# Optimization experiments

Hardware: AMD Instinct MI355X
Metric: run time of the kernel (lower is better)

## Reference

```python
import jax, jax.numpy as jnp
import numpy as np

N = 100000   # nodes
E = 1600000  # edges (avg degree 16)
G = 512      # graphs in batch
IN = 96      # in_channels
H = 128      # hidden_channels
C = 100      # num_classes
ED = 8       # edge_dim
L = 4        # num_layers
EPS_LN = 1e-5


def setup_inputs() -> dict:
    key = jax.random.key(0)
    ks = jax.random.split(key, 24)
    s = 0.05
    d = {
        "x": jax.random.normal(ks[0], (N, IN), jnp.float32),
        "edge_index": jax.random.randint(ks[1], (2, E), 0, N, jnp.int32),
        "batch": jnp.sort(jax.random.randint(ks[2], (N,), 0, G, jnp.int32)),
        "edge_attr": jax.random.normal(ks[3], (E, ED), jnp.float32),
        # edge encoder MLP: Linear(ED,H) -> ReLU -> Linear(H,1)
        "ee_W1": jax.random.normal(ks[4], (ED, H), jnp.float32) * s,
        "ee_b1": jnp.zeros((H,), jnp.float32),
        "ee_W2": jax.random.normal(ks[5], (H, 1), jnp.float32) * s,
        "ee_b2": jnp.zeros((1,), jnp.float32),
        # GCNConv weights (PyG: lin without bias, bias added after aggregation)
        "W0": jax.random.normal(ks[6], (IN, H), jnp.float32) * s,
        "cb0": jnp.zeros((H,), jnp.float32),
        "W1": jax.random.normal(ks[7], (H, H), jnp.float32) * s,
        "cb1": jnp.zeros((H,), jnp.float32),
        "W2": jax.random.normal(ks[8], (H, H), jnp.float32) * s,
        "cb2": jnp.zeros((H,), jnp.float32),
        "W3": jax.random.normal(ks[9], (H, H), jnp.float32) * s,
        "cb3": jnp.zeros((H,), jnp.float32),
        # LayerNorm params
        "g0": jnp.ones((H,), jnp.float32), "be0": jnp.zeros((H,), jnp.float32),
        "g1": jnp.ones((H,), jnp.float32), "be1": jnp.zeros((H,), jnp.float32),
        "g2": jnp.ones((H,), jnp.float32), "be2": jnp.zeros((H,), jnp.float32),
        "g3": jnp.ones((H,), jnp.float32), "be3": jnp.zeros((H,), jnp.float32),
        # residual projection for layer 0 only (IN != H)
        "res_W": jax.random.normal(ks[10], (IN, H), jnp.float32) * s,
        "res_b": jnp.zeros((H,), jnp.float32),
        # head: Linear(2H,H) -> ReLU -> Linear(H,C)
        "hW1": jax.random.normal(ks[11], (2 * H, H), jnp.float32) * s,
        "hb1": jnp.zeros((H,), jnp.float32),
        "hW2": jax.random.normal(ks[12], (H, C), jnp.float32) * s,
        "hb2": jnp.zeros((C,), jnp.float32),
    }
    return d


def _layer_norm(h, g, b):
    mu = jnp.mean(h, axis=-1, keepdims=True)
    var = jnp.mean(jnp.square(h - mu), axis=-1, keepdims=True)
    return g * (h - mu) / jnp.sqrt(var + EPS_LN) + b


def reference(x, edge_index, batch, edge_attr,
              ee_W1, ee_b1, ee_W2, ee_b2,
              W0, cb0, W1, cb1, W2, cb2, W3, cb3,
              g0, be0, g1, be1, g2, be2, g3, be3,
              res_W, res_b, hW1, hb1, hW2, hb2):
    row, col = edge_index[0], edge_index[1]

    # edge weight = softplus(MLP(edge_attr)) + 1e-4  -> [E]
    eh = jax.nn.relu(edge_attr @ ee_W1 + ee_b1)
    ew = jax.nn.softplus((eh @ ee_W2 + ee_b2)[:, 0]) + 1e-4

    # add self loops with weight 1 (PyG GCNConv default)
    loops = jnp.arange(N, dtype=row.dtype)
    row_sl = jnp.concatenate([row, loops])
    col_sl = jnp.concatenate([col, loops])
    ew_sl = jnp.concatenate([ew, jnp.ones((N,), ew.dtype)])

    # symmetric normalization: D^-1/2 A D^-1/2 (deg over target index)
    deg = jax.ops.segment_sum(ew_sl, col_sl, num_segments=N)
    dis = jnp.where(deg > 0, jax.lax.rsqrt(deg), 0.0)
    norm = dis[row_sl] * ew_sl * dis[col_sl]  # [E+N]

    def conv(h, W, b):
        hw = h @ W                                   # [N,H]
        msg = hw[row_sl] * norm[:, None]             # [E+N,H]
        return jax.ops.segment_sum(msg, col_sl, num_segments=N) + b

    Ws = [W0, W1, W2, W3]
    cbs = [cb0, cb1, cb2, cb3]
    gs = [g0, g1, g2, g3]
    bes = [be0, be1, be2, be3]

    hidden = []
    cur = x
    for i in range(L):
        h = conv(cur, Ws[i], cbs[i])
        h = _layer_norm(h, gs[i], bes[i])
        res = cur @ res_W + res_b if i == 0 else cur
        h = jax.nn.relu(h + res)
        # dropout: eval mode -> identity
        hidden.append(h)
        cur = h
    xm = jnp.mean(jnp.stack(hidden, axis=0), axis=0)  # [N,H]

    # meanmax pooling over graphs
    counts = jax.ops.segment_sum(jnp.ones((N,), xm.dtype), batch, num_segments=G)
    gmean = jax.ops.segment_sum(xm, batch, num_segments=G) / jnp.maximum(counts, 1.0)[:, None]
    gmax = jax.ops.segment_max(xm, batch, num_segments=G)
    gmax = jnp.where(jnp.isfinite(gmax), gmax, 0.0)
    g = jnp.concatenate([gmean, gmax], axis=-1)       # [G,2H]

    # head (dropout identity in eval)
    return jax.nn.relu(g @ hW1 + hb1) @ hW2 + hb2     # [G,C]
```

## Files before the change

kernel.cpp:

```cpp
#include <hip/hip_runtime.h>
#include <hip/hip_fp16.h>
#include <math.h>

#define NN 100000
#define EE 1600000
#define GB 512
#define INC 96
#define HH 128
#define CC 100
#define MAXD 64
#define BUCKB 9
#define NBUK 196
#define CAPB 10240
#define EB 4096

typedef __bf16 bf16x8 __attribute__((ext_vector_type(8)));
typedef _Float16 f16x8 __attribute__((ext_vector_type(8)));
typedef float f32x4 __attribute__((ext_vector_type(4)));

__device__ __forceinline__ float unpack_w_f32(unsigned v) {
    return __half2float(__ushort_as_half((unsigned short)(v & 0x7FFFu)));
}
__device__ __forceinline__ __half2 unpack_w_h2(unsigned v) {
    __half h = __ushort_as_half((unsigned short)(v & 0x7FFFu));
    return __halves2half2(h, h);
}

__global__ __launch_bounds__(512) void k_prep(
    const float* __restrict__ W0, const float* __restrict__ resW,
    const float* __restrict__ W1m, const float* __restrict__ W2m, const float* __restrict__ W3m,
    const float* __restrict__ eeW1,
    __half* __restrict__ wt0, __half* __restrict__ wtR,
    __half* __restrict__ wt1, __half* __restrict__ wt2, __half* __restrict__ wt3,
    __bf16* __restrict__ w1f)
{
    int tid = threadIdx.x;
    if (blockIdx.x == 288) {
        int t = tid >> 6, lane = tid & 63;
        int ln15 = lane & 15, quad = lane >> 4;
        bf16x8 v = {};
        if (quad == 0) {
#pragma unroll
            for (int j = 0; j < 8; ++j) v[j] = (__bf16)eeW1[j * 128 + t * 16 + ln15];
        }
        *(bf16x8*)&w1f[(size_t)(t * 64 + lane) * 8] = v;
        return;
    }
    if (tid >= 256) return;
    int idx = blockIdx.x * 256 + tid;
    const float* src; __half* dst; int K, base;
    if (idx < 12288)      { src = W0;   dst = wt0; K = 96;  base = 0; }
    else if (idx < 24576) { src = resW; dst = wtR; K = 96;  base = 12288; }
    else if (idx < 40960) { src = W1m;  dst = wt1; K = 128; base = 24576; }
    else if (idx < 57344) { src = W2m;  dst = wt2; K = 128; base = 40960; }
    else if (idx < 73728) { src = W3m;  dst = wt3; K = 128; base = 57344; }
    else return;
    int l = idx - base;
    int k = l >> 7, n = l & 127;
    dst[(size_t)n * K + k] = __float2half(src[l]);
}

__global__ __launch_bounds__(256) void k_edge_mlp_mfma(
    const float* __restrict__ ea,
    const __bf16* __restrict__ w1f, const float* __restrict__ b1,
    const float* __restrict__ W2, const float* __restrict__ b2,
    __half* __restrict__ ew)
{
    __shared__ float sDot[128];
    int tid = threadIdx.x, wva = tid >> 6, lane = tid & 63;
    int ln15 = lane & 15, quad = lane >> 4;
    int ebase = blockIdx.x * 128 + wva * 32;

    bf16x8 bfr[8];
#pragma unroll
    for (int t = 0; t < 8; ++t) bfr[t] = *(const bf16x8*)&w1f[(size_t)(t * 64 + lane) * 8];

    bf16x8 a0 = {}, a1 = {};
    if (quad == 0) {
        const float* p0 = &ea[(size_t)(ebase + ln15) * 8];
        float4 u0 = *(const float4*)p0, u1 = *(const float4*)(p0 + 4);
        a0[0] = (__bf16)u0.x; a0[1] = (__bf16)u0.y; a0[2] = (__bf16)u0.z; a0[3] = (__bf16)u0.w;
        a0[4] = (__bf16)u1.x; a0[5] = (__bf16)u1.y; a0[6] = (__bf16)u1.z; a0[7] = (__bf16)u1.w;
        const float* p1 = &ea[(size_t)(ebase + 16 + ln15) * 8];
        float4 w0 = *(const float4*)p1, w1v = *(const float4*)(p1 + 4);
        a1[0] = (__bf16)w0.x; a1[1] = (__bf16)w0.y; a1[2] = (__bf16)w0.z; a1[3] = (__bf16)w0.w;
        a1[4] = (__bf16)w1v.x; a1[5] = (__bf16)w1v.y; a1[6] = (__bf16)w1v.z; a1[7] = (__bf16)w1v.w;
    }

    f32x4 d0 = {0.f, 0.f, 0.f, 0.f}, d1 = {0.f, 0.f, 0.f, 0.f};
#pragma unroll
    for (int t = 0; t < 8; ++t) {
        f32x4 z = {0.f, 0.f, 0.f, 0.f};
        f32x4 c0 = __builtin_amdgcn_mfma_f32_16x16x32_bf16(a0, bfr[t], z, 0, 0, 0);
        f32x4 c1 = __builtin_amdgcn_mfma_f32_16x16x32_bf16(a1, bfr[t], z, 0, 0, 0);
        int col = t * 16 + ln15;
        float b1v = b1[col], w2v = W2[col];
#pragma unroll
        for (int r = 0; r < 4; ++r) {
            float v0 = fmaxf(c0[r] + b1v, 0.0f);
            float v1 = fmaxf(c1[r] + b1v, 0.0f);
            d0[r] = fmaf(v0, w2v, d0[r]);
            d1[r] = fmaf(v1, w2v, d1[r]);
        }
    }
#pragma unroll
    for (int o = 1; o < 16; o <<= 1) {
#pragma unroll
        for (int r = 0; r < 4; ++r) {
            d0[r] += __shfl_xor(d0[r], o, 64);
            d1[r] += __shfl_xor(d1[r], o, 64);
        }
    }
    if (ln15 == 0) {
#pragma unroll
        for (int r = 0; r < 4; ++r) {
            sDot[wva * 32 + quad * 4 + r]      = d0[r];
            sDot[wva * 32 + 16 + quad * 4 + r] = d1[r];
        }
    }
    __syncthreads();
    if (tid < 128) {
        int e = blockIdx.x * 128 + tid;
        float x = sDot[tid] + b2[0];
        float sp = (x > 20.0f) ? x : log1pf(expf(x));
        ew[e] = __float2half(sp + 1e-4f);
    }
}

__global__ __launch_bounds__(256) void k_split(const int* __restrict__ ei, const __half* __restrict__ ew,
                                               int* __restrict__ cntB, uint2* __restrict__ barr) {
    __shared__ unsigned hist[NBUK];
    __shared__ unsigned gbase[NBUK];
    __shared__ unsigned short rloc[EB];
    int tid = threadIdx.x;
    for (int b = tid; b < NBUK; b += 256) hist[b] = 0;
    __syncthreads();
    int e0 = blockIdx.x * EB;
#pragma unroll
    for (int j = 0; j < EB / 256; ++j) {
        int e = e0 + j * 256 + tid;
        if (e < EE) {
            int c = ei[EE + e];
            rloc[j * 256 + tid] = (unsigned short)atomicAdd(&hist[c >> BUCKB], 1u);
        }
    }
    __syncthreads();
    for (int b = tid; b < NBUK; b += 256)
        gbase[b] = (hist[b] > 0) ? (unsigned)atomicAdd(&cntB[b], (int)hist[b]) : 0u;
    __syncthreads();
#pragma unroll
    for (int j = 0; j < EB / 256; ++j) {
        int e = e0 + j * 256 + tid;
        if (e < EE) {
            int c = ei[EE + e];
            int b = c >> BUCKB;
            unsigned pos = gbase[b] + rloc[j * 256 + tid];
            if (pos < CAPB) {
                unsigned hb = (unsigned)__half_as_ushort(ew[e]) & 0x7FFFu;
                barr[(size_t)b * CAPB + pos] = make_uint2(((unsigned)c << 15) | hb, (unsigned)ei[e]);
            }
        }
    }
}

__global__ __launch_bounds__(256) void k_build(const int* __restrict__ cntB, const uint2* __restrict__ barr,
                                               unsigned* __restrict__ epack, int* __restrict__ cnt,
                                               float* __restrict__ dis) {
    __shared__ unsigned ncnt[512];
    __shared__ float ndeg[512];
    int tid = threadIdx.x, b = blockIdx.x;
    for (int i = tid; i < 512; i += 256) { ncnt[i] = 0; ndeg[i] = 0.0f; }
    __syncthreads();
    int n0 = b << BUCKB;
    int m = cntB[b]; if (m > CAPB) m = CAPB;
    for (int i = tid; i < m; i += 256) {
        uint2 rec = barr[(size_t)b * CAPB + i];
        int c = (int)(rec.x >> 15);
        int cl = c - n0;
        unsigned rank = atomicAdd(&ncnt[cl], 1u);
        if (rank < MAXD) epack[(size_t)c * MAXD + rank] = (rec.y << 15) | (rec.x & 0x7FFFu);
        atomicAdd(&ndeg[cl], unpack_w_f32(rec.x));
    }
    __syncthreads();
    int nn = NN - n0; if (nn > 512) nn = 512;
    for (int i = tid; i < nn; i += 256) {
        unsigned cc = ncnt[i]; if (cc > MAXD) cc = MAXD;
        cnt[n0 + i] = (int)cc;
        dis[n0 + i] = rsqrtf(1.0f + ndeg[i]);
    }
}

__global__ __launch_bounds__(256) void k_gemm_f16(
    const __half* __restrict__ A, const __half* __restrict__ Bt,
    const float* __restrict__ dis, __half* __restrict__ C, int M, int K)
{
    int tid = threadIdx.x;
    int wv = tid >> 6, lane = tid & 63;
    int ln15 = lane & 15, quad = lane >> 4;
    int m0 = blockIdx.x * 64;
    int n0 = wv * 32;
    f32x4 acc[4][2];
#pragma unroll
    for (int mt = 0; mt < 4; ++mt)
#pragma unroll
        for (int nt = 0; nt < 2; ++nt) acc[mt][nt] = (f32x4){0.f, 0.f, 0.f, 0.f};

    int rowm[4];
#pragma unroll
    for (int mt = 0; mt < 4; ++mt) {
        int r = m0 + mt * 16 + ln15;
        rowm[mt] = r < M ? r : M - 1;
    }
    for (int kc = 0; kc < K; kc += 32) {
        f16x8 af[4], bfr[2];
#pragma unroll
        for (int mt = 0; mt < 4; ++mt)
            af[mt] = *(const f16x8*)&A[(size_t)rowm[mt] * K + kc + quad * 8];
#pragma unroll
        for (int nt = 0; nt < 2; ++nt)
            bfr[nt] = *(const f16x8*)&Bt[(size_t)(n0 + nt * 16 + ln15) * K + kc + quad * 8];
#pragma unroll
        for (int mt = 0; mt < 4; ++mt)
#pragma unroll
            for (int nt = 0; nt < 2; ++nt)
                acc[mt][nt] = __builtin_amdgcn_mfma_f32_16x16x32_f16(af[mt], bfr[nt], acc[mt][nt], 0, 0, 0);
    }
#pragma unroll
    for (int nt = 0; nt < 2; ++nt) {
        int col = n0 + nt * 16 + ln15;
#pragma unroll
        for (int mt = 0; mt < 4; ++mt) {
#pragma unroll
            for (int r = 0; r < 4; ++r) {
                int row = m0 + mt * 16 + quad * 4 + r;
                if (row < M) C[(size_t)row * 128 + col] = __float2half(acc[mt][nt][r] * dis[row]);
            }
        }
    }
}

__global__ __launch_bounds__(256) void k_gemm_dual(
    const float* __restrict__ A, const __half* __restrict__ Bt1, const __half* __restrict__ Bt2,
    const float* __restrict__ bias2, const float* __restrict__ dis,
    __half* __restrict__ C1, __half* __restrict__ C2, int M, int K)
{
    int tid = threadIdx.x;
    int wv = tid >> 6, lane = tid & 63;
    int ln15 = lane & 15, quad = lane >> 4;
    int m0 = blockIdx.x * 64;
    int n0 = wv * 32;
    f32x4 acc1[4][2], acc2[4][2];
#pragma unroll
    for (int mt = 0; mt < 4; ++mt)
#pragma unroll
        for (int nt = 0; nt < 2; ++nt) {
            acc1[mt][nt] = (f32x4){0.f, 0.f, 0.f, 0.f};
            acc2[mt][nt] = (f32x4){0.f, 0.f, 0.f, 0.f};
        }
    int rowm[4];
#pragma unroll
    for (int mt = 0; mt < 4; ++mt) {
        int r = m0 + mt * 16 + ln15;
        rowm[mt] = r < M ? r : M - 1;
    }
    for (int kc = 0; kc < K; kc += 32) {
        f16x8 af[4], bf1[2], bf2[2];
#pragma unroll
        for (int mt = 0; mt < 4; ++mt) {
            const float* ap = &A[(size_t)rowm[mt] * K + kc + quad * 8];
            float4 u0 = *(const float4*)ap, u1 = *(const float4*)(ap + 4);
            af[mt][0] = (_Float16)u0.x; af[mt][1] = (_Float16)u0.y;
            af[mt][2] = (_Float16)u0.z; af[mt][3] = (_Float16)u0.w;
            af[mt][4] = (_Float16)u1.x; af[mt][5] = (_Float16)u1.y;
            af[mt][6] = (_Float16)u1.z; af[mt][7] = (_Float16)u1.w;
        }
#pragma unroll
        for (int nt = 0; nt < 2; ++nt) {
            bf1[nt] = *(const f16x8*)&Bt1[(size_t)(n0 + nt * 16 + ln15) * K + kc + quad * 8];
            bf2[nt] = *(const f16x8*)&Bt2[(size_t)(n0 + nt * 16 + ln15) * K + kc + quad * 8];
        }
#pragma unroll
        for (int mt = 0; mt < 4; ++mt)
#pragma unroll
            for (int nt = 0; nt < 2; ++nt) {
                acc1[mt][nt] = __builtin_amdgcn_mfma_f32_16x16x32_f16(af[mt], bf1[nt], acc1[mt][nt], 0, 0, 0);
                acc2[mt][nt] = __builtin_amdgcn_mfma_f32_16x16x32_f16(af[mt], bf2[nt], acc2[mt][nt], 0, 0, 0);
            }
    }
#pragma unroll
    for (int nt = 0; nt < 2; ++nt) {
        int col = n0 + nt * 16 + ln15;
        float bv2 = bias2[col];
#pragma unroll
        for (int mt = 0; mt < 4; ++mt) {
#pragma unroll
            for (int r = 0; r < 4; ++r) {
                int row = m0 + mt * 16 + quad * 4 + r;
                if (row < M) {
                    C1[(size_t)row * 128 + col] = __float2half(acc1[mt][nt][r] * dis[row]);
                    C2[(size_t)row * 128 + col] = __float2half(acc2[mt][nt][r] + bv2);
                }
            }
        }
    }
}

__global__ __launch_bounds__(256) void k_agg_ln(
    const __half* __restrict__ hw, const float* __restrict__ dis,
    const int* __restrict__ cnt, const unsigned* __restrict__ epack,
    const float* __restrict__ cb, const float* __restrict__ gam,
    const float* __restrict__ bet, const __half* __restrict__ res,
    __half* __restrict__ out, int n)
{
    int wv = threadIdx.x >> 6;
    int lane = threadIdx.x & 63;
    int i = blockIdx.x * 4 + wv;
    if (i >= n) return;
    float di = dis[i];
    __half2 acca = *(const __half2*)&hw[(size_t)i * HH + lane * 2];
    __half2 accb = __halves2half2(__float2half(0.0f), __float2half(0.0f));
    int cn = cnt[i];
    const unsigned* ebase = &epack[(size_t)i * MAXD];
    int k = 0;
    for (; k + 8 <= cn; k += 8) {
        uint4 q0 = *(const uint4*)&ebase[k];
        uint4 q1 = *(const uint4*)&ebase[k + 4];
        __half2 v0 = *(const __half2*)&hw[(size_t)(q0.x >> 15) * HH + lane * 2];
        __half2 v1 = *(const __half2*)&hw[(size_t)(q0.y >> 15) * HH + lane * 2];
        __half2 v2 = *(const __half2*)&hw[(size_t)(q0.z >> 15) * HH + lane * 2];
        __half2 v3 = *(const __half2*)&hw[(size_t)(q0.w >> 15) * HH + lane * 2];
        __half2 v4 = *(const __half2*)&hw[(size_t)(q1.x >> 15) * HH + lane * 2];
        __half2 v5 = *(const __half2*)&hw[(size_t)(q1.y >> 15) * HH + lane * 2];
        __half2 v6 = *(const __half2*)&hw[(size_t)(q1.z >> 15) * HH + lane * 2];
        __half2 v7 = *(const __half2*)&hw[(size_t)(q1.w >> 15) * HH + lane * 2];
        acca = __hfma2(v0, unpack_w_h2(q0.x), acca);
        accb = __hfma2(v4, unpack_w_h2(q1.x), accb);
        acca = __hfma2(v1, unpack_w_h2(q0.y), acca);
        accb = __hfma2(v5, unpack_w_h2(q1.y), accb);
        acca = __hfma2(v2, unpack_w_h2(q0.z), acca);
        accb = __hfma2(v6, unpack_w_h2(q1.z), accb);
        acca = __hfma2(v3, unpack_w_h2(q0.w), acca);
        accb = __hfma2(v7, unpack_w_h2(q1.w), accb);
    }
    for (; k < cn; ++k) {
        unsigned e = ebase[k];
        __half2 v = *(const __half2*)&hw[(size_t)(e >> 15) * HH + lane * 2];
        acca = __hfma2(v, unpack_w_h2(e), acca);
    }
    __half2 acc = __hadd2(acca, accb);
    float2 af = __half22float2(acc);
    float2 cbv = *(const float2*)&cb[lane * 2];
    af.x = fmaf(di, af.x, cbv.x);
    af.y = fmaf(di, af.y, cbv.y);
    float s1 = af.x + af.y;
    float s2 = af.x * af.x + af.y * af.y;
#pragma unroll
    for (int o = 32; o > 0; o >>= 1) {
        s1 += __shfl_xor(s1, o, 64);
        s2 += __shfl_xor(s2, o, 64);
    }
    float mean = s1 * (1.0f / HH);
    float var = fmaxf(s2 * (1.0f / HH) - mean * mean, 0.0f);
    float rstd = rsqrtf(var + 1e-5f);
    float2 gv = *(const float2*)&gam[lane * 2];
    float2 bv = *(const float2*)&bet[lane * 2];
    float2 rv = __half22float2(*(const __half2*)&res[(size_t)i * HH + lane * 2]);
    float hx = fmaxf(fmaf(gv.x, (af.x - mean) * rstd, bv.x) + rv.x, 0.0f);
    float hy = fmaxf(fmaf(gv.y, (af.y - mean) * rstd, bv.y) + rv.y, 0.0f);
    *(__half2*)&out[(size_t)i * HH + lane * 2] = __floats2half2_rn(hx, hy);
}

__global__ __launch_bounds__(512) void k_pool_head(
    const __half* __restrict__ l0, const __half* __restrict__ l1,
    const __half* __restrict__ l2, const __half* __restrict__ l3,
    const int* __restrict__ batch,
    const float* __restrict__ hW1, const float* __restrict__ hb1,
    const float* __restrict__ hW2, const float* __restrict__ hb2,
    float* __restrict__ out, int n)
{
    __shared__ float ssum[8][128];
    __shared__ float smax[8][128];
    __shared__ __align__(16) float sg[256];
    __shared__ __align__(16) float sh[128];
    int g = blockIdx.x, tid = threadIdx.x;
    int grp = tid >> 6, lane = tid & 63;
    int lo = 0, hi = n;
    while (lo < hi) { int m = (lo + hi) >> 1; if (batch[m] < g) lo = m + 1; else hi = m; }
    int start = lo;
    lo = start; hi = n;
    while (lo < hi) { int m = (lo + hi) >> 1; if (batch[m] < g + 1) lo = m + 1; else hi = m; }
    int end = lo;
    float sx = 0.0f, sy = 0.0f, mx = -INFINITY, my = -INFINITY;
    for (int nd = start + grp; nd < end; nd += 8) {
        size_t off = (size_t)nd * HH + lane * 2;
        float2 v0 = __half22float2(*(const __half2*)&l0[off]);
        float2 v1 = __half22float2(*(const __half2*)&l1[off]);
        float2 v2 = __half22float2(*(const __half2*)&l2[off]);
        float2 v3 = __half22float2(*(const __half2*)&l3[off]);
        float vx = (v0.x + v1.x + v2.x + v3.x) * 0.25f;
        float vy = (v0.y + v1.y + v2.y + v3.y) * 0.25f;
        sx += vx; sy += vy;
        mx = fmaxf(mx, vx); my = fmaxf(my, vy);
    }
    ssum[grp][lane * 2] = sx; ssum[grp][lane * 2 + 1] = sy;
    smax[grp][lane * 2] = mx; smax[grp][lane * 2 + 1] = my;
    __syncthreads();
    if (tid < 128) {
        float s = 0.0f, m = -INFINITY;
#pragma unroll
        for (int j = 0; j < 8; ++j) {
            s += ssum[j][tid];
            m = fmaxf(m, smax[j][tid]);
        }
        int cntg = end - start;
        sg[tid] = s / fmaxf((float)cntg, 1.0f);
        sg[128 + tid] = (cntg > 0) ? m : 0.0f;
    }
    __syncthreads();
    if (tid < 128) {
        float h = hb1[tid];
        for (int k = 0; k < 256; ++k) h = fmaf(sg[k], hW1[(size_t)k * 128 + tid], h);
        sh[tid] = fmaxf(h, 0.0f);
    }
    __syncthreads();
    if (tid < 100) {
        float o = hb2[tid];
        for (int k = 0; k < 128; ++k) o = fmaf(sh[k], hW2[(size_t)k * 100 + tid], o);
        out[(size_t)g * 100 + tid] = o;
    }
}

extern "C" void kernel_launch(void* const* d_in, const int* in_sizes, int n_in,
                              void* d_out, int out_size, void* d_ws, size_t ws_size,
                              hipStream_t stream) {
    const float* x     = (const float*)d_in[0];
    const int*   ei    = (const int*)d_in[1];
    const int*   batch = (const int*)d_in[2];
    const float* ea    = (const float*)d_in[3];
    const float* eeW1  = (const float*)d_in[4];
    const float* eeb1  = (const float*)d_in[5];
    const float* eeW2  = (const float*)d_in[6];
    const float* eeb2  = (const float*)d_in[7];
    const float* W[4]  = {(const float*)d_in[8], (const float*)d_in[10], (const float*)d_in[12], (const float*)d_in[14]};
    const float* cb[4] = {(const float*)d_in[9], (const float*)d_in[11], (const float*)d_in[13], (const float*)d_in[15]};
    const float* gm[4] = {(const float*)d_in[16], (const float*)d_in[18], (const float*)d_in[20], (const float*)d_in[22]};
    const float* be[4] = {(const float*)d_in[17], (const float*)d_in[19], (const float*)d_in[21], (const float*)d_in[23]};
    const float* resW  = (const float*)d_in[24];
    const float* resb  = (const float*)d_in[25];
    const float* hW1   = (const float*)d_in[26];
    const float* hb1   = (const float*)d_in[27];
    const float* hW2   = (const float*)d_in[28];
    const float* hb2   = (const float*)d_in[29];
    float* out = (float*)d_out;

    char* w = (char*)d_ws;
    auto alloc = [&](size_t bytes) { void* p = w; w += (bytes + 255) & ~(size_t)255; return p; };
    __half*   ew     = (__half*)  alloc((size_t)EE * 2);
    float*    dis    = (float*)   alloc((size_t)NN * 4);
    int*      cnt    = (int*)     alloc((size_t)NN * 4);
    int*      cntB   = (int*)     alloc((size_t)NBUK * 4);
    uint2*    barr   = (uint2*)   alloc((size_t)NBUK * CAPB * 8);
    unsigned* epack  = (unsigned*)alloc((size_t)(NN * MAXD + 64) * 4);
    __half*   hw     = (__half*)  alloc((size_t)NN * HH * 2);
    __half*   lout[4];
    for (int i = 0; i < 4; ++i) lout[i] = (__half*)alloc((size_t)NN * HH * 2);
    __half*   wt0    = (__half*)  alloc((size_t)INC * HH * 2);
    __half*   wtR    = (__half*)  alloc((size_t)INC * HH * 2);
    __half*   wt1    = (__half*)  alloc((size_t)HH * HH * 2);
    __half*   wt2    = (__half*)  alloc((size_t)HH * HH * 2);
    __half*   wt3    = (__half*)  alloc((size_t)HH * HH * 2);
    __bf16*   w1f    = (__bf16*)  alloc((size_t)8 * 64 * 8 * 2);
    __half*   wtc[4] = {wt0, wt1, wt2, wt3};
    __half*   res0   = lout[1];

    int nblkEdge = EE / 128;
    int nblkSplit = (EE + EB - 1) / EB;
    int nblkGemm = (NN + 63) / 64;

    hipMemsetAsync(cntB, 0, (size_t)NBUK * 4, stream);
    k_prep<<<289, 512, 0, stream>>>(W[0], resW, W[1], W[2], W[3], eeW1,
                                    wt0, wtR, wt1, wt2, wt3, w1f);
    k_edge_mlp_mfma<<<nblkEdge, 256, 0, stream>>>(ea, w1f, eeb1, eeW2, eeb2, ew);
    k_split<<<nblkSplit, 256, 0, stream>>>(ei, ew, cntB, barr);
    k_build<<<NBUK, 256, 0, stream>>>(cntB, barr, epack, cnt, dis);

    k_gemm_dual<<<nblkGemm, 256, 0, stream>>>(x, wt0, wtR, resb, dis, hw, res0, NN, INC);
    k_agg_ln<<<(NN + 3) / 4, 256, 0, stream>>>(hw, dis, cnt, epack,
                                               cb[0], gm[0], be[0], res0, lout[0], NN);
    for (int l = 1; l < 4; ++l) {
        k_gemm_f16<<<nblkGemm, 256, 0, stream>>>(lout[l - 1], wtc[l], dis, hw, NN, HH);
        k_agg_ln<<<(NN + 3) / 4, 256, 0, stream>>>(hw, dis, cnt, epack,
                                                   cb[l], gm[l], be[l], lout[l - 1], lout[l], NN);
    }

    k_pool_head<<<GB, 512, 0, stream>>>(lout[0], lout[1], lout[2], lout[3], batch,
                                        hW1, hb1, hW2, hb2, out, NN);
}
```

Measured before the change: 750.2 us.

## Fuse edge-MLP weight computation into bucket split kernel, drop edge weight buffer

Merges the edge-encoder MFMA kernel with the bucket-split kernel, so each block computes edge weights for 1024 edges into shared memory and builds the bucket histogram in the same pass. This removes the global round trip of the edge-weight array and one kernel launch. The cntB zeroing moves into k_prep, replacing a memset. In-bucket positions now come from shared-memory atomics instead of stored local ranks, which makes edge order within a bucket nondeterministic. The smaller per-block edge chunk means more global atomics on the bucket counters.

```diff
diff --git a/kernel.cpp b/kernel.cpp
--- a/kernel.cpp
+++ b/kernel.cpp
@@ -12,7 +12,7 @@
 #define BUCKB 9
 #define NBUK 196
 #define CAPB 10240
-#define EB 4096
+#define EB 1024
 
 typedef __bf16 bf16x8 __attribute__((ext_vector_type(8)));
 typedef _Float16 f16x8 __attribute__((ext_vector_type(8)));
@@ -32,7 +32,7 @@
     const float* __restrict__ eeW1,
     __half* __restrict__ wt0, __half* __restrict__ wtR,
     __half* __restrict__ wt1, __half* __restrict__ wt2, __half* __restrict__ wt3,
-    __bf16* __restrict__ w1f)
+    __bf16* __restrict__ w1f, int* __restrict__ cntB)
 {
     int tid = threadIdx.x;
     if (blockIdx.x == 288) {
@@ -44,6 +44,7 @@
             for (int j = 0; j < 8; ++j) v[j] = (__bf16)eeW1[j * 128 + t * 16 + ln15];
         }
         *(bf16x8*)&w1f[(size_t)(t * 64 + lane) * 8] = v;
+        if (tid < NBUK) cntB[tid] = 0;
         return;
     }
     if (tid >= 256) return;
@@ -60,93 +61,86 @@
     dst[(size_t)n * K + k] = __float2half(src[l]);
 }
 
-__global__ __launch_bounds__(256) void k_edge_mlp_mfma(
+__global__ __launch_bounds__(256) void k_edge_split(
     const float* __restrict__ ea,
     const __bf16* __restrict__ w1f, const float* __restrict__ b1,
     const float* __restrict__ W2, const float* __restrict__ b2,
-    __half* __restrict__ ew)
+    const int* __restrict__ ei, int* __restrict__ cntB, uint2* __restrict__ barr)
 {
     __shared__ float sDot[128];
+    __shared__ __half ewbuf[EB];
+    __shared__ unsigned hist[NBUK];
+    __shared__ unsigned cur[NBUK];
     int tid = threadIdx.x, wva = tid >> 6, lane = tid & 63;
     int ln15 = lane & 15, quad = lane >> 4;
-    int ebase = blockIdx.x * 128 + wva * 32;
+    for (int b = tid; b < NBUK; b += 256) hist[b] = 0;
 
     bf16x8 bfr[8];
 #pragma unroll
     for (int t = 0; t < 8; ++t) bfr[t] = *(const bf16x8*)&w1f[(size_t)(t * 64 + lane) * 8];
-
-    bf16x8 a0 = {}, a1 = {};
-    if (quad == 0) {
-        const float* p0 = &ea[(size_t)(ebase + ln15) * 8];
-        float4 u0 = *(const float4*)p0, u1 = *(const float4*)(p0 + 4);
-        a0[0] = (__bf16)u0.x; a0[1] = (__bf16)u0.y; a0[2] = (__bf16)u0.z; a0[3] = (__bf16)u0.w;
-        a0[4] = (__bf16)u1.x; a0[5] = (__bf16)u1.y; a0[6] = (__bf16)u1.z; a0[7] = (__bf16)u1.w;
-        const float* p1 = &ea[(size_t)(ebase + 16 + ln15) * 8];
-        float4 w0 = *(const float4*)p1, w1v = *(const float4*)(p1 + 4);
-        a1[0] = (__bf16)w0.x; a1[1] = (__bf16)w0.y; a1[2] = (__bf16)w0.z; a1[3] = (__bf16)w0.w;
-        a1[4] = (__bf16)w1v.x; a1[5] = (__bf16)w1v.y; a1[6] = (__bf16)w1v.z; a1[7] = (__bf16)w1v.w;
-    }
-
-    f32x4 d0 = {0.f, 0.f, 0.f, 0.f}, d1 = {0.f, 0.f, 0.f, 0.f};
-#pragma unroll
-    for (int t = 0; t < 8; ++t) {
-        f32x4 z = {0.f, 0.f, 0.f, 0.f};
-        f32x4 c0 = __builtin_amdgcn_mfma_f32_16x16x32_bf16(a0, bfr[t], z, 0, 0, 0);
-        f32x4 c1 = __builtin_amdgcn_mfma_f32_16x16x32_bf16(a1, bfr[t], z, 0, 0, 0);
-        int col = t * 16 + ln15;
-        float b1v = b1[col], w2v = W2[col];
-#pragma unroll
-        for (int r = 0; r < 4; ++r) {
-            float v0 = fmaxf(c0[r] + b1v, 0.0f);
-            float v1 = fmaxf(c1[r] + b1v, 0.0f);
-            d0[r] = fmaf(v0, w2v, d0[r]);
-            d1[r] = fmaf(v1, w2v, d1[r]);
-        }
-    }
-#pragma unroll
-    for (int o = 1; o < 16; o <<= 1) {
-#pragma unroll
-        for (int r = 0; r < 4; ++r) {
-            d0[r] += __shfl_xor(d0[r], o, 64);
-            d1[r] += __shfl_xor(d1[r], o, 64);
-        }
-    }
-    if (ln15 == 0) {
-#pragma unroll
-        for (int r = 0; r < 4; ++r) {
-            sDot[wva * 32 + quad * 4 + r]      = d0[r];
-            sDot[wva * 32 + 16 + quad * 4 + r] = d1[r];
-        }
-    }
-    __syncthreads();
-    if (tid < 128) {
-        int e = blockIdx.x * 128 + tid;
-        float x = sDot[tid] + b2[0];
-        float sp = (x > 20.0f) ? x : log1pf(expf(x));
-        ew[e] = __float2half(sp + 1e-4f);
-    }
-}
-
-__global__ __launch_bounds__(256) void k_split(const int* __restrict__ ei, const __half* __restrict__ ew,
-                                               int* __restrict__ cntB, uint2* __restrict__ barr) {
-    __shared__ unsigned hist[NBUK];
-    __shared__ unsigned gbase[NBUK];
-    __shared__ unsigned short rloc[EB];
-    int tid = threadIdx.x;
-    for (int b = tid; b < NBUK; b += 256) hist[b] = 0;
-    __syncthreads();
+    __syncthreads();
+
     int e0 = blockIdx.x * EB;
-#pragma unroll
-    for (int j = 0; j < EB / 256; ++j) {
-        int e = e0 + j * 256 + tid;
-        if (e < EE) {
-            int c = ei[EE + e];
-            rloc[j * 256 + tid] = (unsigned short)atomicAdd(&hist[c >> BUCKB], 1u);
-        }
-    }
-    __syncthreads();
+#pragma unroll 1
+    for (int tile = 0; tile < EB / 128; ++tile) {
+        int tbase = e0 + tile * 128;
+        if (tbase < EE) {
+            int eb2 = tbase + wva * 32;
+            bf16x8 a0 = {}, a1 = {};
+            if (quad == 0) {
+                const float* p0 = &ea[(size_t)(eb2 + ln15) * 8];
+                float4 u0 = *(const float4*)p0, u1 = *(const float4*)(p0 + 4);
+                a0[0] = (__bf16)u0.x; a0[1] = (__bf16)u0.y; a0[2] = (__bf16)u0.z; a0[3] = (__bf16)u0.w;
+                a0[4] = (__bf16)u1.x; a0[5] = (__bf16)u1.y; a0[6] = (__bf16)u1.z; a0[7] = (__bf16)u1.w;
+                const float* p1 = &ea[(size_t)(eb2 + 16 + ln15) * 8];
+                float4 w0 = *(const float4*)p1, w1v = *(const float4*)(p1 + 4);
+                a1[0] = (__bf16)w0.x; a1[1] = (__bf16)w0.y; a1[2] = (__bf16)w0.z; a1[3] = (__bf16)w0.w;
+                a1[4] = (__bf16)w1v.x; a1[5] = (__bf16)w1v.y; a1[6] = (__bf16)w1v.z; a1[7] = (__bf16)w1v.w;
+            }
+            f32x4 d0 = {0.f, 0.f, 0.f, 0.f}, d1 = {0.f, 0.f, 0.f, 0.f};
+#pragma unroll
+            for (int t = 0; t < 8; ++t) {
+                f32x4 z = {0.f, 0.f, 0.f, 0.f};
+                f32x4 c0 = __builtin_amdgcn_mfma_f32_16x16x32_bf16(a0, bfr[t], z, 0, 0, 0);
+                f32x4 c1 = __builtin_amdgcn_mfma_f32_16x16x32_bf16(a1, bfr[t], z, 0, 0, 0);
+                int col = t * 16 + ln15;
+                float b1v = b1[col], w2v = W2[col];
+#pragma unroll
+                for (int r = 0; r < 4; ++r) {
+                    float v0 = fmaxf(c0[r] + b1v, 0.0f);
+                    float v1 = fmaxf(c1[r] + b1v, 0.0f);
+                    d0[r] = fmaf(v0, w2v, d0[r]);
+                    d1[r] = fmaf(v1, w2v, d1[r]);
+                }
+            }
+#pragma unroll
+            for (int o = 1; o < 16; o <<= 1) {
+#pragma unroll
+                for (int r = 0; r < 4; ++r) {
+                    d0[r] += __shfl_xor(d0[r], o, 64);
+                    d1[r] += __shfl_xor(d1[r], o, 64);
+                }
+            }
+            if (ln15 == 0) {
+#pragma unroll
+                for (int r = 0; r < 4; ++r) {
+                    sDot[wva * 32 + quad * 4 + r]      = d0[r];
+                    sDot[wva * 32 + 16 + quad * 4 + r] = d1[r];
+                }
+            }
+            __syncthreads();
+            if (tid < 128) {
+                int e = tbase + tid;
+                float xv = sDot[tid] + b2[0];
+                float sp = (xv > 20.0f) ? xv : log1pf(expf(xv));
+                ewbuf[tile * 128 + tid] = __float2half(sp + 1e-4f);
+                atomicAdd(&hist[ei[EE + e] >> BUCKB], 1u);
+            }
+        }
+        __syncthreads();
+    }
     for (int b = tid; b < NBUK; b += 256)
-        gbase[b] = (hist[b] > 0) ? (unsigned)atomicAdd(&cntB[b], (int)hist[b]) : 0u;
+        cur[b] = (hist[b] > 0) ? (unsigned)atomicAdd(&cntB[b], (int)hist[b]) : 0u;
     __syncthreads();
 #pragma unroll
     for (int j = 0; j < EB / 256; ++j) {
@@ -154,9 +148,9 @@
         if (e < EE) {
             int c = ei[EE + e];
             int b = c >> BUCKB;
-            unsigned pos = gbase[b] + rloc[j * 256 + tid];
+            unsigned pos = atomicAdd(&cur[b], 1u);
             if (pos < CAPB) {
-                unsigned hb = (unsigned)__half_as_ushort(ew[e]) & 0x7FFFu;
+                unsigned hb = (unsigned)__half_as_ushort(ewbuf[j * 256 + tid]) & 0x7FFFu;
                 barr[(size_t)b * CAPB + pos] = make_uint2(((unsigned)c << 15) | hb, (unsigned)ei[e]);
             }
         }
@@ -455,7 +449,6 @@
 
     char* w = (char*)d_ws;
     auto alloc = [&](size_t bytes) { void* p = w; w += (bytes + 255) & ~(size_t)255; return p; };
-    __half*   ew     = (__half*)  alloc((size_t)EE * 2);
     float*    dis    = (float*)   alloc((size_t)NN * 4);
     int*      cnt    = (int*)     alloc((size_t)NN * 4);
     int*      cntB   = (int*)     alloc((size_t)NBUK * 4);
@@ -473,15 +466,12 @@
     __half*   wtc[4] = {wt0, wt1, wt2, wt3};
     __half*   res0   = lout[1];
 
-    int nblkEdge = EE / 128;
-    int nblkSplit = (EE + EB - 1) / EB;
+    int nblkEdge = (EE + EB - 1) / EB;
     int nblkGemm = (NN + 63) / 64;
 
-    hipMemsetAsync(cntB, 0, (size_t)NBUK * 4, stream);
     k_prep<<<289, 512, 0, stream>>>(W[0], resW, W[1], W[2], W[3], eeW1,
-                                    wt0, wtR, wt1, wt2, wt3, w1f);
-    k_edge_mlp_mfma<<<nblkEdge, 256, 0, stream>>>(ea, w1f, eeb1, eeW2, eeb2, ew);
-    k_split<<<nblkSplit, 256, 0, stream>>>(ei, ew, cntB, barr);
+                                    wt0, wtR, wt1, wt2, wt3, w1f, cntB);
+    k_edge_split<<<nblkEdge, 256, 0, stream>>>(ea, w1f, eeb1, eeW2, eeb2, ei, cntB, barr);
     k_build<<<NBUK, 256, 0, stream>>>(cntB, barr, epack, cnt, dis);
 
     k_gemm_dual<<<nblkGemm, 256, 0, stream>>>(x, wt0, wtR, resb, dis, hw, res0, NN, INC);
```

After: 760.4 us. About the same (+1.4%).
